# Kernel tuning notes

Measured on AMD Instinct MI355X. Metric: run time of the kernel, lower is better.

## Reference

```python
import jax, jax.numpy as jnp
import numpy as np

N_NODES = 100000
N_EDGES = 3200000
D_IN = 256
D_OUT = 256


def setup_inputs() -> dict:
    key = jax.random.key(0)
    k1, k2, k3, k4, k5 = jax.random.split(key, 5)
    x = jax.random.normal(k1, (N_NODES, D_IN), dtype=jnp.float32)
    # xavier-uniform-like init for weight
    limit = float(np.sqrt(6.0 / (D_IN + D_OUT)))
    weight = jax.random.uniform(k2, (D_IN, D_OUT), dtype=jnp.float32, minval=-limit, maxval=limit)
    edge_val = jax.random.uniform(k3, (N_EDGES,), dtype=jnp.float32)
    edge_row = jax.random.randint(k4, (N_EDGES,), 0, N_NODES, dtype=jnp.int32)
    edge_col = jax.random.randint(k5, (N_EDGES,), 0, N_NODES, dtype=jnp.int32)
    return {"x": x, "weight": weight, "edge_val": edge_val,
            "edge_row": edge_row, "edge_col": edge_col}


def reference(x, weight, edge_val, edge_row, edge_col):
    # dropout p=0.0 -> identity
    support = x @ weight                                  # [N, D_OUT]
    # spmm: out[r] += val * support[c] for each edge (r, c, val)
    msgs = support[edge_col] * edge_val[:, None]          # [E, D_OUT]
    out = jax.ops.segment_sum(msgs, edge_row, num_segments=N_NODES)
    return jax.nn.relu(out)
```

## Files before the change

### kernel.cpp

```cpp
#include <hip/hip_runtime.h>

#define N_NODES 100000
#define N_EDGES 3200000
#define D 256
#define OVF_MAX 8192

#define NB1 98
#define CAPB1 34816
#define CHUNK 6144
#define NBLK_A ((N_EDGES + CHUNK - 1) / CHUNK)

#define NQ (NB1 * 4)
#define QROWS 256
#define QCAP 9216

#define CAST_BLOCKS 6250
#define GEMM_BLOCKS (N_NODES / 16)
#define SPMM_HALF 50000

typedef __attribute__((ext_vector_type(8))) short bf16x8;
typedef __attribute__((ext_vector_type(4))) float f32x4;

__device__ unsigned short g_wtp[(size_t)16 * 8 * 64 * 8];
__device__ int   g_b1cur[NB1 * 16];
__device__ int   g_novf;
__device__ int   g_ovf_row[OVF_MAX];
__device__ int2  g_ovf_edge[OVF_MAX];

__device__ unsigned short g_xb_fb[(size_t)N_NODES * D];
__device__ unsigned       g_y_fb[(size_t)N_NODES * (D / 2)];
__device__ int2           g_binned_fb[(size_t)NB1 * CAPB1];
__device__ int2           g_grp_fb[(size_t)NQ * QCAP];
__device__ int2           g_rofs_fb[(size_t)NQ * QROWS];

__device__ __forceinline__ unsigned short f2bf(float f) {
    unsigned u = __float_as_uint(f);
    unsigned r = u + 0x7fffu + ((u >> 16) & 1u);
    return (unsigned short)(r >> 16);
}

__global__ void setup_kernel(const float* __restrict__ W) {
    const int tid = threadIdx.x;
    if (blockIdx.x < 64) {
        int pb = (blockIdx.x * 256 + tid) * 4;
        #pragma unroll
        for (int j = 0; j < 4; ++j) {
            int p    = pb + j;
            int i8   = p & 7;
            int lane = (p >> 3) & 63;
            int s    = (p >> 9) & 7;
            int nt   = p >> 12;
            int n = nt * 16 + (lane & 15);
            int k = s * 32 + (lane >> 4) * 8 + i8;
            g_wtp[p] = f2bf(W[(size_t)k * D + n]);
        }
    }
    if (blockIdx.x == 0) {
        for (int i = tid; i < NB1 * 16; i += 256) g_b1cur[i] = 0;
        if (tid == 0) g_novf = 0;
    }
}

__launch_bounds__(256)
__global__ void binA_kernel(const float* __restrict__ edge_val,
                            const int* __restrict__ edge_row,
                            const int* __restrict__ edge_col,
                            int2* __restrict__ binned) {
    __shared__ int2 rec[CHUNK];
    __shared__ unsigned char bid[CHUNK];
    __shared__ int cnt[NB1];
    __shared__ int pre[NB1 + 1];
    __shared__ int bas[NB1];
    const int tid = threadIdx.x;
    const int e0 = blockIdx.x * CHUNK;

    for (int k = tid; k < NB1; k += 256) cnt[k] = 0;
    __syncthreads();
    #pragma unroll
    for (int j = 0; j < CHUNK / 256; ++j) {
        int e = e0 + tid + j * 256;
        if (e < N_EDGES) atomicAdd(&cnt[edge_row[e] >> 10], 1);
    }
    __syncthreads();
    if (tid == 0) {
        int run = 0;
        for (int k = 0; k < NB1; ++k) { pre[k] = run; run += cnt[k]; }
        pre[NB1] = run;
    }
    __syncthreads();
    for (int k = tid; k < NB1; k += 256)
        bas[k] = cnt[k] ? atomicAdd(&g_b1cur[k * 16], cnt[k]) : 0;
    __syncthreads();
    for (int k = tid; k < NB1; k += 256) cnt[k] = 0;
    __syncthreads();
    #pragma unroll
    for (int j = 0; j < CHUNK / 256; ++j) {
        int e = e0 + tid + j * 256;
        if (e < N_EDGES) {
            int r = edge_row[e];
            int k = r >> 10;
            int o = atomicAdd(&cnt[k], 1);
            int pos = pre[k] + o;
            int2 pk;
            pk.x = edge_col[e] | ((r & 1023) << 17);
            pk.y = __float_as_int(edge_val[e]);
            rec[pos] = pk;
            bid[pos] = (unsigned char)k;
        }
    }
    __syncthreads();
    const int total = pre[NB1];
    for (int i = tid; i < total; i += 256) {
        int k = bid[i];
        int dest = bas[k] + (i - pre[k]);
        int2 pk = rec[i];
        if (dest < CAPB1) {
            binned[(size_t)k * CAPB1 + dest] = pk;
        } else {
            int o = atomicAdd(&g_novf, 1);
            if (o < OVF_MAX) {
                g_ovf_row[o] = (k << 10) | (pk.x >> 17);
                int2 ov; ov.x = pk.x & 0x1FFFF; ov.y = pk.y;
                g_ovf_edge[o] = ov;
            }
        }
    }
}

__launch_bounds__(512)
__global__ void binB_sort_kernel(const int2* __restrict__ binned,
                                 int2* __restrict__ grp,
                                 int2* __restrict__ rofs) {
    __shared__ int2 srec[QCAP];
    __shared__ int cnt[QROWS];
    __shared__ int ofs[QROWS];
    __shared__ int cur[QROWS];
    const int tid = threadIdx.x;
    const int b   = blockIdx.x >> 2;
    const int qtr = blockIdx.x & 3;

    const int n = min(g_b1cur[b * 16], CAPB1);
    const int2* src = &binned[(size_t)b * CAPB1];

    if (tid < QROWS) { cnt[tid] = 0; cur[tid] = 0; }
    __syncthreads();
    for (int i = tid; i < n; i += 512) {
        int rl = src[i].x >> 17;
        if ((rl >> 8) == qtr) atomicAdd(&cnt[rl & 255], 1);
    }
    __syncthreads();
    if (tid < QROWS) {
        int s = 0;
        for (int j = 0; j < tid; ++j) s += cnt[j];
        ofs[tid] = s;
    }
    __syncthreads();
    for (int i = tid; i < n; i += 512) {
        int2 pk = src[i];
        int rl = pk.x >> 17;
        if ((rl >> 8) == qtr) {
            int r8 = rl & 255;
            int p = ofs[r8] + atomicAdd(&cur[r8], 1);
            int2 o2; o2.x = pk.x & 0x1FFFF; o2.y = pk.y;
            if (p < QCAP) {
                srec[p] = o2;
            } else {
                int o = atomicAdd(&g_novf, 1);
                if (o < OVF_MAX) {
                    g_ovf_row[o] = (b << 10) + (qtr << 8) + r8;
                    g_ovf_edge[o] = o2;
                }
            }
        }
    }
    __syncthreads();
    const int total = min(ofs[QROWS - 1] + cnt[QROWS - 1], QCAP);
    int2* dst = &grp[(size_t)blockIdx.x * QCAP];
    for (int i = tid; i < total; i += 512) dst[i] = srec[i];
    if (tid < QROWS) {
        int s = min(ofs[tid], QCAP);
        int e = min(ofs[tid] + cnt[tid], QCAP);
        int2 oc; oc.x = s; oc.y = e - s;
        rofs[(size_t)blockIdx.x * QROWS + tid] = oc;
    }
}

__launch_bounds__(256)
__global__ void cast_kernel(const float* __restrict__ x,
                            unsigned short* __restrict__ xb) {
    const size_t blockBase = (size_t)blockIdx.x * 4096;
    const int tid = threadIdx.x;
    #pragma unroll
    for (int j = 0; j < 4; ++j) {
        size_t idx = blockBase + (size_t)(j * 256 + tid) * 4;
        float4 f = *(const float4*)&x[idx];
        unsigned short o[4];
        o[0] = f2bf(f.x); o[1] = f2bf(f.y);
        o[2] = f2bf(f.z); o[3] = f2bf(f.w);
        *(uint2*)&xb[idx] = *(const uint2*)o;
    }
}

__launch_bounds__(128)
__global__ void spmm_kernel(const int2* __restrict__ grp,
                            const int2* __restrict__ rofs,
                            const unsigned short* __restrict__ xbp,
                            unsigned* __restrict__ y,
                            int rowBase) {
    const int r = rowBase + blockIdx.x;
    const int t = threadIdx.x;
    const int blk = r >> 8;
    const int2 oc = rofs[(size_t)blk * QROWS + (r & 255)];
    const int deg = oc.y;
    const long long* rowp =
        (const long long*)&grp[(size_t)blk * QCAP + oc.x];
    const unsigned* xb = (const unsigned*)xbp;

    float a0 = 0.f, a1 = 0.f;
    int i = 0;
    for (; i + 3 < deg; i += 4) {
        long long q0 = __builtin_nontemporal_load(&rowp[i]);
        long long q1 = __builtin_nontemporal_load(&rowp[i + 1]);
        long long q2 = __builtin_nontemporal_load(&rowp[i + 2]);
        long long q3 = __builtin_nontemporal_load(&rowp[i + 3]);
        unsigned p0 = xb[(size_t)(int)q0 * (D / 2) + t];
        unsigned p1 = xb[(size_t)(int)q1 * (D / 2) + t];
        unsigned p2 = xb[(size_t)(int)q2 * (D / 2) + t];
        unsigned p3 = xb[(size_t)(int)q3 * (D / 2) + t];
        float v0 = __int_as_float((int)(q0 >> 32));
        float v1 = __int_as_float((int)(q1 >> 32));
        float v2 = __int_as_float((int)(q2 >> 32));
        float v3 = __int_as_float((int)(q3 >> 32));
        a0 += v0 * __uint_as_float(p0 << 16);
        a1 += v0 * __uint_as_float(p0 & 0xffff0000u);
        a0 += v1 * __uint_as_float(p1 << 16);
        a1 += v1 * __uint_as_float(p1 & 0xffff0000u);
        a0 += v2 * __uint_as_float(p2 << 16);
        a1 += v2 * __uint_as_float(p2 & 0xffff0000u);
        a0 += v3 * __uint_as_float(p3 << 16);
        a1 += v3 * __uint_as_float(p3 & 0xffff0000u);
    }
    for (; i < deg; ++i) {
        long long q0 = __builtin_nontemporal_load(&rowp[i]);
        float v0 = __int_as_float((int)(q0 >> 32));
        unsigned p0 = xb[(size_t)(int)q0 * (D / 2) + t];
        a0 += v0 * __uint_as_float(p0 << 16);
        a1 += v0 * __uint_as_float(p0 & 0xffff0000u);
    }
    const int novf = min(g_novf, OVF_MAX);
    if (novf > 0) {
        for (int j = 0; j < novf; ++j) {
            if (g_ovf_row[j] == r) {
                int2 e0 = g_ovf_edge[j];
                float v0 = __int_as_float(e0.y);
                unsigned p0 = xb[(size_t)e0.x * (D / 2) + t];
                a0 += v0 * __uint_as_float(p0 << 16);
                a1 += v0 * __uint_as_float(p0 & 0xffff0000u);
            }
        }
    }
    y[(size_t)r * (D / 2) + t] =
        (unsigned)f2bf(a0) | ((unsigned)f2bf(a1) << 16);
}

__launch_bounds__(256)
__global__ void gemm_kernel(const unsigned short* __restrict__ Yb,
                            float* __restrict__ out) {
    __shared__ float tile[4][16][68];
    const int g    = blockIdx.x;
    const int wave = threadIdx.x >> 6;
    const int lane = threadIdx.x & 63;
    const int m0   = g * 16;
    const int n0   = wave * 64;
    const int lm   = lane & 15;
    const int q    = lane >> 4;

    f32x4 acc0 = {}, acc1 = {}, acc2 = {}, acc3 = {};

    #pragma unroll
    for (int s = 0; s < 8; ++s) {
        bf16x8 av = *(const bf16x8*)&Yb[(size_t)(m0 + lm) * D + s * 32 + q * 8];
        const unsigned short* bp =
            &g_wtp[((size_t)(wave * 4) * 8 + s) * 512 + lane * 8];
        bf16x8 b0 = *(const bf16x8*)&bp[0 * 4096];
        bf16x8 b1 = *(const bf16x8*)&bp[1 * 4096];
        bf16x8 b2 = *(const bf16x8*)&bp[2 * 4096];
        bf16x8 b3 = *(const bf16x8*)&bp[3 * 4096];
        acc0 = __builtin_amdgcn_mfma_f32_16x16x32_bf16(av, b0, acc0, 0, 0, 0);
        acc1 = __builtin_amdgcn_mfma_f32_16x16x32_bf16(av, b1, acc1, 0, 0, 0);
        acc2 = __builtin_amdgcn_mfma_f32_16x16x32_bf16(av, b2, acc2, 0, 0, 0);
        acc3 = __builtin_amdgcn_mfma_f32_16x16x32_bf16(av, b3, acc3, 0, 0, 0);
    }

    #pragma unroll
    for (int r = 0; r < 4; ++r) {
        tile[wave][q * 4 + r][ 0 + lm] = acc0[r];
        tile[wave][q * 4 + r][16 + lm] = acc1[r];
        tile[wave][q * 4 + r][32 + lm] = acc2[r];
        tile[wave][q * 4 + r][48 + lm] = acc3[r];
    }
    const int row  = lane >> 2;
    const int cseg = (lane & 3) * 16;
    float ov[16];
    #pragma unroll
    for (int j = 0; j < 16; ++j)
        ov[j] = fmaxf(tile[wave][row][cseg + j], 0.f);
    float* dst = &out[(size_t)(m0 + row) * D + n0 + cseg];
    #pragma unroll
    for (int j = 0; j < 4; ++j)
        __builtin_nontemporal_store(*(const f32x4*)&ov[j * 4], (f32x4*)&dst[j * 4]);
}

#define XB_BYTES   ((size_t)N_NODES * D * 2)
#define Y_BYTES    ((size_t)N_NODES * D * 2)
#define BIN_BYTES  ((size_t)NB1 * CAPB1 * 8)
#define GRP_BYTES  ((size_t)NQ * QCAP * 8)
#define ROFS_BYTES ((size_t)NQ * QROWS * 8)
#define ALIGNUP(v) (((v) + 255) & ~(size_t)255)

extern "C" void kernel_launch(void* const* d_in, const int* in_sizes, int n_in,
                              void* d_out, int out_size, void* d_ws, size_t ws_size,
                              hipStream_t stream) {
    const float* x        = (const float*)d_in[0];
    const float* weight   = (const float*)d_in[1];
    const float* edge_val = (const float*)d_in[2];
    const int*   edge_row = (const int*)d_in[3];
    const int*   edge_col = (const int*)d_in[4];
    float* out = (float*)d_out;

    static void* s_xb = nullptr; static void* s_y = nullptr;
    static void* s_bin = nullptr; static void* s_grp = nullptr;
    static void* s_rofs = nullptr;
    if (!s_xb) {
        hipGetSymbolAddress(&s_xb,   HIP_SYMBOL(g_xb_fb));
        hipGetSymbolAddress(&s_y,    HIP_SYMBOL(g_y_fb));
        hipGetSymbolAddress(&s_bin,  HIP_SYMBOL(g_binned_fb));
        hipGetSymbolAddress(&s_grp,  HIP_SYMBOL(g_grp_fb));
        hipGetSymbolAddress(&s_rofs, HIP_SYMBOL(g_rofs_fb));
    }
    unsigned short* xb;  unsigned* y;  int2* binned;  int2* grp;  int2* rofs;
    const size_t need = ALIGNUP(XB_BYTES) + ALIGNUP(Y_BYTES) +
                        ALIGNUP(BIN_BYTES) + ALIGNUP(GRP_BYTES) +
                        ALIGNUP(ROFS_BYTES);
    if (d_ws && ws_size >= need) {
        char* p = (char*)d_ws;
        xb     = (unsigned short*)p; p += ALIGNUP(XB_BYTES);
        y      = (unsigned*)p;       p += ALIGNUP(Y_BYTES);
        binned = (int2*)p;           p += ALIGNUP(BIN_BYTES);
        grp    = (int2*)p;           p += ALIGNUP(GRP_BYTES);
        rofs   = (int2*)p;
    } else {
        xb     = (unsigned short*)s_xb;
        y      = (unsigned*)s_y;
        binned = (int2*)s_bin;
        grp    = (int2*)s_grp;
        rofs   = (int2*)s_rofs;
    }

    setup_kernel<<<64, 256, 0, stream>>>(weight);
    binA_kernel<<<NBLK_A, 256, 0, stream>>>(edge_val, edge_row, edge_col, binned);
    binB_sort_kernel<<<NQ, 512, 0, stream>>>(binned, grp, rofs);
    cast_kernel<<<CAST_BLOCKS, 256, 0, stream>>>(x, xb);
    spmm_kernel<<<SPMM_HALF, 128, 0, stream>>>(grp, rofs, xb, y, 0);
    spmm_kernel<<<SPMM_HALF, 128, 0, stream>>>(grp, rofs, xb, y, SPMM_HALF);
    gemm_kernel<<<GEMM_BLOCKS, 256, 0, stream>>>((const unsigned short*)y, out);
}
```

Baseline: 620.1 us.

## Fuse cast with weight pack, halve binning chunk, parallel-scan row offsets

Merges the x-to-bf16 cast and the weight packing into one launch and moves the counter reset to a memset, removing one kernel launch. The binning kernel uses a smaller chunk so more blocks run, and splits its shared-memory histogram per half-block to reduce atomic contention. The sort kernel goes to 1024 threads and replaces the serial per-thread prefix loop with a Hillis-Steele scan. Smaller chunks raise the number of global atomic reservations, and the scan adds extra barriers.

```diff
diff --git a/kernel.cpp b/kernel.cpp
--- a/kernel.cpp
+++ b/kernel.cpp
@@ -7,7 +7,7 @@
 
 #define NB1 98
 #define CAPB1 34816
-#define CHUNK 6144
+#define CHUNK 3072
 #define NBLK_A ((N_EDGES + CHUNK - 1) / CHUNK)
 
 #define NQ (NB1 * 4)
@@ -15,6 +15,7 @@
 #define QCAP 9216
 
 #define CAST_BLOCKS 6250
+#define PACK_BLOCKS 64
 #define GEMM_BLOCKS (N_NODES / 16)
 #define SPMM_HALF 50000
 
@@ -22,10 +23,10 @@
 typedef __attribute__((ext_vector_type(4))) float f32x4;
 
 __device__ unsigned short g_wtp[(size_t)16 * 8 * 64 * 8];
-__device__ int   g_b1cur[NB1 * 16];
-__device__ int   g_novf;
+__device__ int   g_ctr[NB1 * 16 + 16];
 __device__ int   g_ovf_row[OVF_MAX];
 __device__ int2  g_ovf_edge[OVF_MAX];
+#define NOVF_IDX (NB1 * 16)
 
 __device__ unsigned short g_xb_fb[(size_t)N_NODES * D];
 __device__ unsigned       g_y_fb[(size_t)N_NODES * (D / 2)];
@@ -39,10 +40,25 @@
     return (unsigned short)(r >> 16);
 }
 
-__global__ void setup_kernel(const float* __restrict__ W) {
+__launch_bounds__(256)
+__global__ void cast_pack_kernel(const float* __restrict__ x,
+                                 const float* __restrict__ W,
+                                 unsigned short* __restrict__ xb) {
     const int tid = threadIdx.x;
-    if (blockIdx.x < 64) {
-        int pb = (blockIdx.x * 256 + tid) * 4;
+    const int b = blockIdx.x;
+    if (b < CAST_BLOCKS) {
+        const size_t blockBase = (size_t)b * 4096;
+        #pragma unroll
+        for (int j = 0; j < 4; ++j) {
+            size_t idx = blockBase + (size_t)(j * 256 + tid) * 4;
+            float4 f = *(const float4*)&x[idx];
+            unsigned short o[4];
+            o[0] = f2bf(f.x); o[1] = f2bf(f.y);
+            o[2] = f2bf(f.z); o[3] = f2bf(f.w);
+            *(uint2*)&xb[idx] = *(const uint2*)o;
+        }
+    } else {
+        int pb = ((b - CAST_BLOCKS) * 256 + tid) * 4;
         #pragma unroll
         for (int j = 0; j < 4; ++j) {
             int p    = pb + j;
@@ -55,10 +71,6 @@
             g_wtp[p] = f2bf(W[(size_t)k * D + n]);
         }
     }
-    if (blockIdx.x == 0) {
-        for (int i = tid; i < NB1 * 16; i += 256) g_b1cur[i] = 0;
-        if (tid == 0) g_novf = 0;
-    }
 }
 
 __launch_bounds__(256)
@@ -68,30 +80,39 @@
                             int2* __restrict__ binned) {
     __shared__ int2 rec[CHUNK];
     __shared__ unsigned char bid[CHUNK];
-    __shared__ int cnt[NB1];
+    __shared__ int c2[2][NB1];
+    __shared__ int snap0[NB1];
     __shared__ int pre[NB1 + 1];
     __shared__ int bas[NB1];
     const int tid = threadIdx.x;
+    const int half = tid >> 7;
     const int e0 = blockIdx.x * CHUNK;
 
-    for (int k = tid; k < NB1; k += 256) cnt[k] = 0;
+    for (int k = tid; k < 2 * NB1; k += 256) ((int*)c2)[k] = 0;
     __syncthreads();
     #pragma unroll
     for (int j = 0; j < CHUNK / 256; ++j) {
         int e = e0 + tid + j * 256;
-        if (e < N_EDGES) atomicAdd(&cnt[edge_row[e] >> 10], 1);
+        if (e < N_EDGES) atomicAdd(&c2[half][edge_row[e] >> 10], 1);
     }
     __syncthreads();
     if (tid == 0) {
         int run = 0;
-        for (int k = 0; k < NB1; ++k) { pre[k] = run; run += cnt[k]; }
+        for (int k = 0; k < NB1; ++k) {
+            int c0 = c2[0][k];
+            snap0[k] = c0;
+            pre[k] = run;
+            run += c0 + c2[1][k];
+        }
         pre[NB1] = run;
     }
     __syncthreads();
-    for (int k = tid; k < NB1; k += 256)
-        bas[k] = cnt[k] ? atomicAdd(&g_b1cur[k * 16], cnt[k]) : 0;
-    __syncthreads();
-    for (int k = tid; k < NB1; k += 256) cnt[k] = 0;
+    for (int k = tid; k < NB1; k += 256) {
+        int tot = snap0[k] + c2[1][k];
+        bas[k] = tot ? atomicAdd(&g_ctr[k * 16], tot) : 0;
+    }
+    __syncthreads();
+    for (int k = tid; k < 2 * NB1; k += 256) ((int*)c2)[k] = 0;
     __syncthreads();
     #pragma unroll
     for (int j = 0; j < CHUNK / 256; ++j) {
@@ -99,8 +120,8 @@
         if (e < N_EDGES) {
             int r = edge_row[e];
             int k = r >> 10;
-            int o = atomicAdd(&cnt[k], 1);
-            int pos = pre[k] + o;
+            int o = atomicAdd(&c2[half][k], 1);
+            int pos = pre[k] + (half ? snap0[k] : 0) + o;
             int2 pk;
             pk.x = edge_col[e] | ((r & 1023) << 17);
             pk.y = __float_as_int(edge_val[e]);
@@ -117,7 +138,7 @@
         if (dest < CAPB1) {
             binned[(size_t)k * CAPB1 + dest] = pk;
         } else {
-            int o = atomicAdd(&g_novf, 1);
+            int o = atomicAdd(&g_ctr[NOVF_IDX], 1);
             if (o < OVF_MAX) {
                 g_ovf_row[o] = (k << 10) | (pk.x >> 17);
                 int2 ov; ov.x = pk.x & 0x1FFFF; ov.y = pk.y;
@@ -127,35 +148,42 @@
     }
 }
 
-__launch_bounds__(512)
+__launch_bounds__(1024)
 __global__ void binB_sort_kernel(const int2* __restrict__ binned,
                                  int2* __restrict__ grp,
                                  int2* __restrict__ rofs) {
     __shared__ int2 srec[QCAP];
     __shared__ int cnt[QROWS];
+    __shared__ int scn[QROWS];
     __shared__ int ofs[QROWS];
     __shared__ int cur[QROWS];
     const int tid = threadIdx.x;
     const int b   = blockIdx.x >> 2;
     const int qtr = blockIdx.x & 3;
 
-    const int n = min(g_b1cur[b * 16], CAPB1);
+    const int n = min(g_ctr[b * 16], CAPB1);
     const int2* src = &binned[(size_t)b * CAPB1];
 
     if (tid < QROWS) { cnt[tid] = 0; cur[tid] = 0; }
     __syncthreads();
-    for (int i = tid; i < n; i += 512) {
+    for (int i = tid; i < n; i += 1024) {
         int rl = src[i].x >> 17;
         if ((rl >> 8) == qtr) atomicAdd(&cnt[rl & 255], 1);
     }
     __syncthreads();
-    if (tid < QROWS) {
-        int s = 0;
-        for (int j = 0; j < tid; ++j) s += cnt[j];
-        ofs[tid] = s;
-    }
-    __syncthreads();
-    for (int i = tid; i < n; i += 512) {
+    if (tid < QROWS) scn[tid] = cnt[tid];
+    __syncthreads();
+    #pragma unroll
+    for (int d = 1; d < QROWS; d <<= 1) {
+        int v = 0;
+        if (tid < QROWS) { v = scn[tid]; if (tid >= d) v += scn[tid - d]; }
+        __syncthreads();
+        if (tid < QROWS) scn[tid] = v;
+        __syncthreads();
+    }
+    if (tid < QROWS) ofs[tid] = scn[tid] - cnt[tid];
+    __syncthreads();
+    for (int i = tid; i < n; i += 1024) {
         int2 pk = src[i];
         int rl = pk.x >> 17;
         if ((rl >> 8) == qtr) {
@@ -165,7 +193,7 @@
             if (p < QCAP) {
                 srec[p] = o2;
             } else {
-                int o = atomicAdd(&g_novf, 1);
+                int o = atomicAdd(&g_ctr[NOVF_IDX], 1);
                 if (o < OVF_MAX) {
                     g_ovf_row[o] = (b << 10) + (qtr << 8) + r8;
                     g_ovf_edge[o] = o2;
@@ -174,30 +202,14 @@
         }
     }
     __syncthreads();
-    const int total = min(ofs[QROWS - 1] + cnt[QROWS - 1], QCAP);
+    const int total = min(scn[QROWS - 1], QCAP);
     int2* dst = &grp[(size_t)blockIdx.x * QCAP];
-    for (int i = tid; i < total; i += 512) dst[i] = srec[i];
+    for (int i = tid; i < total; i += 1024) dst[i] = srec[i];
     if (tid < QROWS) {
         int s = min(ofs[tid], QCAP);
         int e = min(ofs[tid] + cnt[tid], QCAP);
         int2 oc; oc.x = s; oc.y = e - s;
         rofs[(size_t)blockIdx.x * QROWS + tid] = oc;
-    }
-}
-
-__launch_bounds__(256)
-__global__ void cast_kernel(const float* __restrict__ x,
-                            unsigned short* __restrict__ xb) {
-    const size_t blockBase = (size_t)blockIdx.x * 4096;
-    const int tid = threadIdx.x;
-    #pragma unroll
-    for (int j = 0; j < 4; ++j) {
-        size_t idx = blockBase + (size_t)(j * 256 + tid) * 4;
-        float4 f = *(const float4*)&x[idx];
-        unsigned short o[4];
-        o[0] = f2bf(f.x); o[1] = f2bf(f.y);
-        o[2] = f2bf(f.z); o[3] = f2bf(f.w);
-        *(uint2*)&xb[idx] = *(const uint2*)o;
     }
 }
 
@@ -247,7 +259,7 @@
         a0 += v0 * __uint_as_float(p0 << 16);
         a1 += v0 * __uint_as_float(p0 & 0xffff0000u);
     }
-    const int novf = min(g_novf, OVF_MAX);
+    const int novf = min(g_ctr[NOVF_IDX], OVF_MAX);
     if (novf > 0) {
         for (int j = 0; j < novf; ++j) {
             if (g_ovf_row[j] == r) {
@@ -330,13 +342,14 @@
 
     static void* s_xb = nullptr; static void* s_y = nullptr;
     static void* s_bin = nullptr; static void* s_grp = nullptr;
-    static void* s_rofs = nullptr;
+    static void* s_rofs = nullptr; static void* s_ctr = nullptr;
     if (!s_xb) {
         hipGetSymbolAddress(&s_xb,   HIP_SYMBOL(g_xb_fb));
         hipGetSymbolAddress(&s_y,    HIP_SYMBOL(g_y_fb));
         hipGetSymbolAddress(&s_bin,  HIP_SYMBOL(g_binned_fb));
         hipGetSymbolAddress(&s_grp,  HIP_SYMBOL(g_grp_fb));
         hipGetSymbolAddress(&s_rofs, HIP_SYMBOL(g_rofs_fb));
+        hipGetSymbolAddress(&s_ctr,  HIP_SYMBOL(g_ctr));
     }
     unsigned short* xb;  unsigned* y;  int2* binned;  int2* grp;  int2* rofs;
     const size_t need = ALIGNUP(XB_BYTES) + ALIGNUP(Y_BYTES) +
@@ -357,10 +370,10 @@
         rofs   = (int2*)s_rofs;
     }
 
-    setup_kernel<<<64, 256, 0, stream>>>(weight);
+    hipMemsetAsync(s_ctr, 0, (size_t)(NB1 * 16 + 16) * 4, stream);
+    cast_pack_kernel<<<CAST_BLOCKS + PACK_BLOCKS, 256, 0, stream>>>(x, weight, xb);
     binA_kernel<<<NBLK_A, 256, 0, stream>>>(edge_val, edge_row, edge_col, binned);
-    binB_sort_kernel<<<NQ, 512, 0, stream>>>(binned, grp, rofs);
-    cast_kernel<<<CAST_BLOCKS, 256, 0, stream>>>(x, xb);
+    binB_sort_kernel<<<NQ, 1024, 0, stream>>>(binned, grp, rofs);
     spmm_kernel<<<SPMM_HALF, 128, 0, stream>>>(grp, rofs, xb, y, 0);
     spmm_kernel<<<SPMM_HALF, 128, 0, stream>>>(grp, rofs, xb, y, SPMM_HALF);
     gemm_kernel<<<GEMM_BLOCKS, 256, 0, stream>>>((const unsigned short*)y, out);
```

Result: faster. 567.0 us (-8.6%).
